# Performance work log

Hardware: AMD Instinct MI355X
Metric: run time of the kernel (lower is better)

## Reference

```python
import jax, jax.numpy as jnp
import numpy as np

DELTA = 0.2  # margin from __init__
EPS = 1e-8   # torch cosine_similarity eps


def setup_inputs() -> dict:
    key = jax.random.key(0)
    k1, k2, k3 = jax.random.split(key, 3)
    B, D, N = 4096, 1024, 8192
    return {
        "q": jax.random.normal(k1, (B, D), dtype=jnp.float32),
        "k": jax.random.normal(k2, (B, D), dtype=jnp.float32),
        "queue": jax.random.normal(k3, (N, D), dtype=jnp.float32),
    }


def _l2_normalize(x):
    # matches torch cosine_similarity clamping: norm clamped to eps
    n = jnp.maximum(jnp.linalg.norm(x, axis=-1, keepdims=True), EPS)
    return x / n


def reference(q, k, queue):
    qn = _l2_normalize(q)          # [B, D]
    kn = _l2_normalize(k)          # [B, D]
    queuen = _l2_normalize(queue)  # [N, D]
    pos = jnp.sum(qn * kn, axis=-1)                 # [B] cos(q_i, k_i)
    neg = jnp.einsum("bd,nd->bn", qn, queuen)       # [B, N] cos(q_i, queue_j)
    hinge = jax.nn.relu(DELTA - pos[:, None] + neg)  # [B, N]
    return jnp.sum(hinge)
```

## Files before the change

### kernel.cpp

```cpp
#include <hip/hip_runtime.h>

#define B_ROWS 4096
#define N_ROWS 8192
#define DDIM   1024
#define DELTA_M 0.2f
#define EPSF    1e-8f

#define BK3 32
#define NW  (DDIM / BK3)

typedef short bf16x8 __attribute__((ext_vector_type(8)));
typedef float f32x4 __attribute__((ext_vector_type(4)));

__device__ inline unsigned short f32_to_bf16(float f) {
    unsigned int u = __float_as_uint(f);
    u += 0x7FFFu + ((u >> 16) & 1u);
    return (unsigned short)(u >> 16);
}

__device__ inline void load_lds16(const void* g, void* l) {
    __builtin_amdgcn_global_load_lds(
        (const __attribute__((address_space(1))) void*)g,
        (__attribute__((address_space(3))) void*)l,
        16, 0, 0);
}

__global__ __launch_bounds__(256)
void norm_kernel(const float* __restrict__ q, const float* __restrict__ k,
                 const float* __restrict__ queue,
                 unsigned short* __restrict__ qn,
                 unsigned short* __restrict__ qun,
                 float* __restrict__ pos, float* __restrict__ out) {
    const int tid  = threadIdx.x;
    const int lane = tid & 63;
    const int wave = tid >> 6;
    const int row  = blockIdx.x * 4 + wave;
    if (blockIdx.x == 0 && tid == 0) *out = 0.f;

    if (row < B_ROWS) {
        const float4* qr = reinterpret_cast<const float4*>(q + (size_t)row * DDIM);
        const float4* kr = reinterpret_cast<const float4*>(k + (size_t)row * DDIM);
        float4 a[4], b[4];
        #pragma unroll
        for (int j = 0; j < 4; ++j) a[j] = qr[lane + j * 64];
        #pragma unroll
        for (int j = 0; j < 4; ++j) b[j] = kr[lane + j * 64];
        float s11 = 0.f, s22 = 0.f, s12 = 0.f;
        #pragma unroll
        for (int j = 0; j < 4; ++j) {
            s11 += a[j].x * a[j].x + a[j].y * a[j].y + a[j].z * a[j].z + a[j].w * a[j].w;
            s22 += b[j].x * b[j].x + b[j].y * b[j].y + b[j].z * b[j].z + b[j].w * b[j].w;
            s12 += a[j].x * b[j].x + a[j].y * b[j].y + a[j].z * b[j].z + a[j].w * b[j].w;
        }
        #pragma unroll
        for (int off = 1; off < 64; off <<= 1) {
            s11 += __shfl_xor(s11, off);
            s22 += __shfl_xor(s22, off);
            s12 += __shfl_xor(s12, off);
        }
        const float inv1 = 1.0f / fmaxf(sqrtf(s11), EPSF);
        const float inv2 = 1.0f / fmaxf(sqrtf(s22), EPSF);
        if (lane == 0) pos[row] = s12 * inv1 * inv2;
        ushort4* orow = reinterpret_cast<ushort4*>(qn + (size_t)row * DDIM);
        #pragma unroll
        for (int j = 0; j < 4; ++j) {
            ushort4 o;
            o.x = f32_to_bf16(a[j].x * inv1);
            o.y = f32_to_bf16(a[j].y * inv1);
            o.z = f32_to_bf16(a[j].z * inv1);
            o.w = f32_to_bf16(a[j].w * inv1);
            orow[lane + j * 64] = o;
        }
    } else {
        const int r2 = row - B_ROWS;
        const float4* qr = reinterpret_cast<const float4*>(queue + (size_t)r2 * DDIM);
        float4 a[4];
        #pragma unroll
        for (int j = 0; j < 4; ++j) a[j] = qr[lane + j * 64];
        float s11 = 0.f;
        #pragma unroll
        for (int j = 0; j < 4; ++j)
            s11 += a[j].x * a[j].x + a[j].y * a[j].y + a[j].z * a[j].z + a[j].w * a[j].w;
        #pragma unroll
        for (int off = 1; off < 64; off <<= 1) s11 += __shfl_xor(s11, off);
        const float inv1 = 1.0f / fmaxf(sqrtf(s11), EPSF);
        ushort4* orow = reinterpret_cast<ushort4*>(qun + (size_t)r2 * DDIM);
        #pragma unroll
        for (int j = 0; j < 4; ++j) {
            ushort4 o;
            o.x = f32_to_bf16(a[j].x * inv1);
            o.y = f32_to_bf16(a[j].y * inv1);
            o.z = f32_to_bf16(a[j].z * inv1);
            o.w = f32_to_bf16(a[j].w * inv1);
            orow[lane + j * 64] = o;
        }
    }
}

struct Frags { bf16x8 a[8]; bf16x8 b[4]; };

__device__ __forceinline__ void ld_frags(const unsigned char* buf, int aBase, int bBase,
                                         Frags& f) {
    #pragma unroll
    for (int fm = 0; fm < 8; ++fm)
        f.a[fm] = *reinterpret_cast<const bf16x8*>(&buf[aBase + fm * 1024]);
    #pragma unroll
    for (int fn = 0; fn < 4; ++fn)
        f.b[fn] = *reinterpret_cast<const bf16x8*>(&buf[16384 + bBase + fn * 1024]);
}

__device__ __forceinline__ void do_mfma(const Frags& f, f32x4 (&acc)[8][4]) {
    __builtin_amdgcn_s_setprio(1);
    #pragma unroll
    for (int fm = 0; fm < 8; ++fm)
        #pragma unroll
        for (int fn = 0; fn < 4; ++fn)
            acc[fm][fn] = __builtin_amdgcn_mfma_f32_16x16x32_bf16(
                f.a[fm], f.b[fn], acc[fm][fn], 0, 0, 0);
    __builtin_amdgcn_s_setprio(0);
}

__device__ __forceinline__ void stage(const unsigned short* sA0, const unsigned short* sA1,
                                      const unsigned short* sB0, const unsigned short* sB1,
                                      int k0, unsigned char* buf, int t16) {
    load_lds16(sA0 + k0, buf + t16);
    load_lds16(sA1 + k0, buf + 8192 + t16);
    load_lds16(sB0 + k0, buf + 16384 + t16);
    load_lds16(sB1 + k0, buf + 24576 + t16);
}

template<bool STG, int WE>
__device__ __forceinline__ void window(int T, unsigned char* lds,
    Frags& use, Frags& nxt,
    const unsigned short* sA0, const unsigned short* sA1,
    const unsigned short* sB0, const unsigned short* sB1,
    int aBase, int bBase, int t16, f32x4 (&acc)[8][4]) {

    ld_frags(lds + ((T + 1) % 3) * 32768, aBase, bBase, nxt);
    if (STG)
        stage(sA0, sA1, sB0, sB1, (T + 3) * BK3, lds + (T % 3) * 32768, t16);
    do_mfma(use, acc);
    if (WE == 4)      asm volatile("s_waitcnt vmcnt(4)" ::: "memory");
    else if (WE == 0) asm volatile("s_waitcnt vmcnt(0)" ::: "memory");
    asm volatile("s_waitcnt lgkmcnt(0)" ::: "memory");
    __builtin_amdgcn_sched_barrier(0);
    if (WE >= 0) __builtin_amdgcn_s_barrier();
}

__global__ __launch_bounds__(512, 2)
void gemm_hinge(const unsigned short* __restrict__ A,
                const unsigned short* __restrict__ Bq,
                const float* __restrict__ pos,
                float* __restrict__ out) {
    __shared__ __align__(16) unsigned char lds[98304];

    const int tid  = threadIdx.x;
    const int lane = tid & 63;
    const int wave = tid >> 6;

    const int bid = blockIdx.x;
    const int x   = bid & 7;
    const int idx = bid >> 3;
    const int bm = ((x & 1) * 8 + (idx & 7)) * 256;
    const int bn = ((x >> 1) * 8 + (idx >> 3)) * 256;

    const int wr = wave >> 2, wc = wave & 3;
    const int ln15 = lane & 15, kq = lane >> 4;
    const int kqoff = (kq * 16) ^ (((ln15 >> 1) & 3) << 4);
    const int aBase = wr * 8192 + ln15 * 64 + kqoff;
    const int bBase = wc * 4096 + ln15 * 64 + kqoff;

    const int t16 = tid * 16;
    const int d0 = t16, d1 = t16 + 8192;
    const int l0 = d0 ^ (((d0 >> 7) & 3) << 4);
    const int l1 = d1 ^ (((d1 >> 7) & 3) << 4);
    const int sr0 = l0 >> 6, sc0 = (l0 & 63) >> 1;
    const int sr1 = l1 >> 6, sc1 = (l1 & 63) >> 1;
    const unsigned short* sA0 = A  + (size_t)(bm + sr0) * DDIM + sc0;
    const unsigned short* sA1 = A  + (size_t)(bm + sr1) * DDIM + sc1;
    const unsigned short* sB0 = Bq + (size_t)(bn + sr0) * DDIM + sc0;
    const unsigned short* sB1 = Bq + (size_t)(bn + sr1) * DDIM + sc1;

    f32x4 acc[8][4];
    #pragma unroll
    for (int fm = 0; fm < 8; ++fm)
        #pragma unroll
        for (int fn = 0; fn < 4; ++fn)
            acc[fm][fn] = (f32x4){0.f, 0.f, 0.f, 0.f};

    Frags fA, fB;

    stage(sA0, sA1, sB0, sB1, 0,       lds,         t16);
    stage(sA0, sA1, sB0, sB1, BK3,     lds + 32768, t16);
    stage(sA0, sA1, sB0, sB1, 2 * BK3, lds + 65536, t16);
    asm volatile("s_waitcnt vmcnt(8)" ::: "memory");
    __builtin_amdgcn_sched_barrier(0);
    __builtin_amdgcn_s_barrier();
    ld_frags(lds, aBase, bBase, fA);
    asm volatile("s_waitcnt vmcnt(4) lgkmcnt(0)" ::: "memory");
    __builtin_amdgcn_sched_barrier(0);
    __builtin_amdgcn_s_barrier();

    #pragma unroll 1
    for (int T = 0; T < 28; T += 2) {
        window<true, 4>(T,     lds, fA, fB, sA0, sA1, sB0, sB1, aBase, bBase, t16, acc);
        window<true, 4>(T + 1, lds, fB, fA, sA0, sA1, sB0, sB1, aBase, bBase, t16, acc);
    }
    window<true,  4>(28, lds, fA, fB, sA0, sA1, sB0, sB1, aBase, bBase, t16, acc);
    window<false, 0>(29, lds, fB, fA, sA0, sA1, sB0, sB1, aBase, bBase, t16, acc);
    window<false,-1>(30, lds, fA, fB, sA0, sA1, sB0, sB1, aBase, bBase, t16, acc);
    do_mfma(fB, acc);

    float lsum = 0.f;
    #pragma unroll
    for (int fm = 0; fm < 8; ++fm) {
        const float4 p4 = *reinterpret_cast<const float4*>(
            pos + bm + wr * 128 + fm * 16 + kq * 4);
        const float pj[4] = {p4.x, p4.y, p4.z, p4.w};
        #pragma unroll
        for (int fn = 0; fn < 4; ++fn)
            #pragma unroll
            for (int j = 0; j < 4; ++j)
                lsum += fmaxf(DELTA_M - pj[j] + acc[fm][fn][j], 0.f);
    }
    #pragma unroll
    for (int off = 32; off; off >>= 1) lsum += __shfl_down(lsum, off);
    __syncthreads();
    float* red = reinterpret_cast<float*>(lds);
    if (lane == 0) red[wave] = lsum;
    __syncthreads();
    if (tid == 0) {
        float s = 0.f;
        #pragma unroll
        for (int w = 0; w < 8; ++w) s += red[w];
        atomicAdd(out, s);
    }
}

extern "C" void kernel_launch(void* const* d_in, const int* in_sizes, int n_in,
                              void* d_out, int out_size, void* d_ws, size_t ws_size,
                              hipStream_t stream) {
    const float* q     = (const float*)d_in[0];
    const float* k     = (const float*)d_in[1];
    const float* queue = (const float*)d_in[2];
    float* out = (float*)d_out;

    unsigned short* qn  = (unsigned short*)d_ws;
    unsigned short* qun = qn + (size_t)B_ROWS * DDIM;
    float* pos = (float*)(qun + (size_t)N_ROWS * DDIM);

    norm_kernel<<<(B_ROWS + N_ROWS) / 4, 256, 0, stream>>>(q, k, queue, qn, qun, pos, out);
    gemm_hinge<<<(B_ROWS / 256) * (N_ROWS / 256), 512, 0, stream>>>(qn, qun, pos, out);
}
```

Baseline: 155.4 us.

## Switch GEMM operands to FP8 with pre-tiled fragment layout from norm kernel

Result: faster. 148.1 us (-4.7%).

```diff
diff --git a/kernel.cpp b/kernel.cpp
--- a/kernel.cpp
+++ b/kernel.cpp
@@ -6,17 +6,11 @@
 #define DELTA_M 0.2f
 #define EPSF    1e-8f
 
-#define BK3 32
-#define NW  (DDIM / BK3)
-
-typedef short bf16x8 __attribute__((ext_vector_type(8)));
+#define NW 32
+#define PANEL (256 * DDIM)
+
 typedef float f32x4 __attribute__((ext_vector_type(4)));
-
-__device__ inline unsigned short f32_to_bf16(float f) {
-    unsigned int u = __float_as_uint(f);
-    u += 0x7FFFu + ((u >> 16) & 1u);
-    return (unsigned short)(u >> 16);
-}
+typedef unsigned long long u64;
 
 __device__ inline void load_lds16(const void* g, void* l) {
     __builtin_amdgcn_global_load_lds(
@@ -25,11 +19,17 @@
         16, 0, 0);
 }
 
+__device__ inline unsigned int pk4(float a, float b, float c, float d) {
+    int v = __builtin_amdgcn_cvt_pk_fp8_f32(a, b, 0, false);
+    v = __builtin_amdgcn_cvt_pk_fp8_f32(c, d, v, true);
+    return (unsigned int)v;
+}
+
 __global__ __launch_bounds__(256)
 void norm_kernel(const float* __restrict__ q, const float* __restrict__ k,
                  const float* __restrict__ queue,
-                 unsigned short* __restrict__ qn,
-                 unsigned short* __restrict__ qun,
+                 unsigned char* __restrict__ qn,
+                 unsigned char* __restrict__ qun,
                  float* __restrict__ pos, float* __restrict__ out) {
     const int tid  = threadIdx.x;
     const int lane = tid & 63;
@@ -42,9 +42,9 @@
         const float4* kr = reinterpret_cast<const float4*>(k + (size_t)row * DDIM);
         float4 a[4], b[4];
         #pragma unroll
-        for (int j = 0; j < 4; ++j) a[j] = qr[lane + j * 64];
-        #pragma unroll
-        for (int j = 0; j < 4; ++j) b[j] = kr[lane + j * 64];
+        for (int j = 0; j < 4; ++j) a[j] = qr[lane * 4 + j];
+        #pragma unroll
+        for (int j = 0; j < 4; ++j) b[j] = kr[lane * 4 + j];
         float s11 = 0.f, s22 = 0.f, s12 = 0.f;
         #pragma unroll
         for (int j = 0; j < 4; ++j) {
@@ -61,22 +61,23 @@
         const float inv1 = 1.0f / fmaxf(sqrtf(s11), EPSF);
         const float inv2 = 1.0f / fmaxf(sqrtf(s22), EPSF);
         if (lane == 0) pos[row] = s12 * inv1 * inv2;
-        ushort4* orow = reinterpret_cast<ushort4*>(qn + (size_t)row * DDIM);
-        #pragma unroll
-        for (int j = 0; j < 4; ++j) {
-            ushort4 o;
-            o.x = f32_to_bf16(a[j].x * inv1);
-            o.y = f32_to_bf16(a[j].y * inv1);
-            o.z = f32_to_bf16(a[j].z * inv1);
-            o.w = f32_to_bf16(a[j].w * inv1);
-            orow[lane + j * 64] = o;
-        }
+        u64 g0 = (u64)pk4(a[0].x * inv1, a[0].y * inv1, a[0].z * inv1, a[0].w * inv1)
+               | ((u64)pk4(a[1].x * inv1, a[1].y * inv1, a[1].z * inv1, a[1].w * inv1) << 32);
+        u64 g1 = (u64)pk4(a[2].x * inv1, a[2].y * inv1, a[2].z * inv1, a[2].w * inv1)
+               | ((u64)pk4(a[3].x * inv1, a[3].y * inv1, a[3].z * inv1, a[3].w * inv1) << 32);
+        const size_t base = (size_t)(row >> 8) * PANEL
+                          + (size_t)(lane >> 1) * 8192
+                          + (size_t)((row >> 4) & 15) * 512
+                          + (size_t)((lane & 1) * 2) * 128
+                          + (size_t)(row & 15) * 8;
+        *reinterpret_cast<u64*>(qn + base)       = g0;
+        *reinterpret_cast<u64*>(qn + base + 128) = g1;
     } else {
         const int r2 = row - B_ROWS;
         const float4* qr = reinterpret_cast<const float4*>(queue + (size_t)r2 * DDIM);
         float4 a[4];
         #pragma unroll
-        for (int j = 0; j < 4; ++j) a[j] = qr[lane + j * 64];
+        for (int j = 0; j < 4; ++j) a[j] = qr[lane * 4 + j];
         float s11 = 0.f;
         #pragma unroll
         for (int j = 0; j < 4; ++j)
@@ -84,29 +85,30 @@
         #pragma unroll
         for (int off = 1; off < 64; off <<= 1) s11 += __shfl_xor(s11, off);
         const float inv1 = 1.0f / fmaxf(sqrtf(s11), EPSF);
-        ushort4* orow = reinterpret_cast<ushort4*>(qun + (size_t)r2 * DDIM);
-        #pragma unroll
-        for (int j = 0; j < 4; ++j) {
-            ushort4 o;
-            o.x = f32_to_bf16(a[j].x * inv1);
-            o.y = f32_to_bf16(a[j].y * inv1);
-            o.z = f32_to_bf16(a[j].z * inv1);
-            o.w = f32_to_bf16(a[j].w * inv1);
-            orow[lane + j * 64] = o;
-        }
-    }
-}
-
-struct Frags { bf16x8 a[8]; bf16x8 b[4]; };
-
-__device__ __forceinline__ void ld_frags(const unsigned char* buf, int aBase, int bBase,
+        u64 g0 = (u64)pk4(a[0].x * inv1, a[0].y * inv1, a[0].z * inv1, a[0].w * inv1)
+               | ((u64)pk4(a[1].x * inv1, a[1].y * inv1, a[1].z * inv1, a[1].w * inv1) << 32);
+        u64 g1 = (u64)pk4(a[2].x * inv1, a[2].y * inv1, a[2].z * inv1, a[2].w * inv1)
+               | ((u64)pk4(a[3].x * inv1, a[3].y * inv1, a[3].z * inv1, a[3].w * inv1) << 32);
+        const size_t base = (size_t)(r2 >> 8) * PANEL
+                          + (size_t)(lane >> 1) * 8192
+                          + (size_t)((r2 >> 4) & 15) * 512
+                          + (size_t)((lane & 1) * 2) * 128
+                          + (size_t)(r2 & 15) * 8;
+        *reinterpret_cast<u64*>(qun + base)       = g0;
+        *reinterpret_cast<u64*>(qun + base + 128) = g1;
+    }
+}
+
+struct Frags { long long a[8]; long long b[4]; };
+
+__device__ __forceinline__ void ld_frags(const unsigned char* buf, int aOff, int bOff,
                                          Frags& f) {
     #pragma unroll
     for (int fm = 0; fm < 8; ++fm)
-        f.a[fm] = *reinterpret_cast<const bf16x8*>(&buf[aBase + fm * 1024]);
+        f.a[fm] = *reinterpret_cast<const long long*>(buf + aOff + fm * 512);
     #pragma unroll
     for (int fn = 0; fn < 4; ++fn)
-        f.b[fn] = *reinterpret_cast<const bf16x8*>(&buf[16384 + bBase + fn * 1024]);
+        f.b[fn] = *reinterpret_cast<const long long*>(buf + 8192 + bOff + fn * 512);
 }
 
 __device__ __forceinline__ void do_mfma(const Frags& f, f32x4 (&acc)[8][4]) {
@@ -115,32 +117,25 @@
     for (int fm = 0; fm < 8; ++fm)
         #pragma unroll
         for (int fn = 0; fn < 4; ++fn)
-            acc[fm][fn] = __builtin_amdgcn_mfma_f32_16x16x32_bf16(
+            acc[fm][fn] = __builtin_amdgcn_mfma_f32_16x16x32_fp8_fp8(
                 f.a[fm], f.b[fn], acc[fm][fn], 0, 0, 0);
     __builtin_amdgcn_s_setprio(0);
-}
-
-__device__ __forceinline__ void stage(const unsigned short* sA0, const unsigned short* sA1,
-                                      const unsigned short* sB0, const unsigned short* sB1,
-                                      int k0, unsigned char* buf, int t16) {
-    load_lds16(sA0 + k0, buf + t16);
-    load_lds16(sA1 + k0, buf + 8192 + t16);
-    load_lds16(sB0 + k0, buf + 16384 + t16);
-    load_lds16(sB1 + k0, buf + 24576 + t16);
 }
 
 template<bool STG, int WE>
 __device__ __forceinline__ void window(int T, unsigned char* lds,
     Frags& use, Frags& nxt,
-    const unsigned short* sA0, const unsigned short* sA1,
-    const unsigned short* sB0, const unsigned short* sB1,
-    int aBase, int bBase, int t16, f32x4 (&acc)[8][4]) {
-
-    ld_frags(lds + ((T + 1) % 3) * 32768, aBase, bBase, nxt);
-    if (STG)
-        stage(sA0, sA1, sB0, sB1, (T + 3) * BK3, lds + (T % 3) * 32768, t16);
+    const unsigned char* srcA, const unsigned char* srcB,
+    int aOff, int bOff, int t16, f32x4 (&acc)[8][4]) {
+
+    ld_frags(lds + ((T + 1) % 3) * 16384, aOff, bOff, nxt);
+    if (STG) {
+        unsigned char* buf = lds + (T % 3) * 16384;
+        load_lds16(srcA + (T + 3) * 8192, buf + t16);
+        load_lds16(srcB + (T + 3) * 8192, buf + 8192 + t16);
+    }
     do_mfma(use, acc);
-    if (WE == 4)      asm volatile("s_waitcnt vmcnt(4)" ::: "memory");
+    if (WE == 2)      asm volatile("s_waitcnt vmcnt(2)" ::: "memory");
     else if (WE == 0) asm volatile("s_waitcnt vmcnt(0)" ::: "memory");
     asm volatile("s_waitcnt lgkmcnt(0)" ::: "memory");
     __builtin_amdgcn_sched_barrier(0);
@@ -148,11 +143,11 @@
 }
 
 __global__ __launch_bounds__(512, 2)
-void gemm_hinge(const unsigned short* __restrict__ A,
-                const unsigned short* __restrict__ Bq,
+void gemm_hinge(const unsigned char* __restrict__ A,
+                const unsigned char* __restrict__ Bq,
                 const float* __restrict__ pos,
                 float* __restrict__ out) {
-    __shared__ __align__(16) unsigned char lds[98304];
+    __shared__ __align__(16) unsigned char lds[49152];
 
     const int tid  = threadIdx.x;
     const int lane = tid & 63;
@@ -161,25 +156,16 @@
     const int bid = blockIdx.x;
     const int x   = bid & 7;
     const int idx = bid >> 3;
-    const int bm = ((x & 1) * 8 + (idx & 7)) * 256;
-    const int bn = ((x >> 1) * 8 + (idx >> 3)) * 256;
+    const int bm = ((x & 1) * 8 + (idx & 7));
+    const int bn = ((x >> 1) * 8 + (idx >> 3));
 
     const int wr = wave >> 2, wc = wave & 3;
-    const int ln15 = lane & 15, kq = lane >> 4;
-    const int kqoff = (kq * 16) ^ (((ln15 >> 1) & 3) << 4);
-    const int aBase = wr * 8192 + ln15 * 64 + kqoff;
-    const int bBase = wc * 4096 + ln15 * 64 + kqoff;
+    const int aOff = wr * 4096 + lane * 8;
+    const int bOff = wc * 2048 + lane * 8;
 
     const int t16 = tid * 16;
-    const int d0 = t16, d1 = t16 + 8192;
-    const int l0 = d0 ^ (((d0 >> 7) & 3) << 4);
-    const int l1 = d1 ^ (((d1 >> 7) & 3) << 4);
-    const int sr0 = l0 >> 6, sc0 = (l0 & 63) >> 1;
-    const int sr1 = l1 >> 6, sc1 = (l1 & 63) >> 1;
-    const unsigned short* sA0 = A  + (size_t)(bm + sr0) * DDIM + sc0;
-    const unsigned short* sA1 = A  + (size_t)(bm + sr1) * DDIM + sc1;
-    const unsigned short* sB0 = Bq + (size_t)(bn + sr0) * DDIM + sc0;
-    const unsigned short* sB1 = Bq + (size_t)(bn + sr1) * DDIM + sc1;
+    const unsigned char* srcA = A  + (size_t)bm * PANEL + t16;
+    const unsigned char* srcB = Bq + (size_t)bn * PANEL + t16;
 
     f32x4 acc[8][4];
     #pragma unroll
@@ -190,32 +176,34 @@
 
     Frags fA, fB;
 
-    stage(sA0, sA1, sB0, sB1, 0,       lds,         t16);
-    stage(sA0, sA1, sB0, sB1, BK3,     lds + 32768, t16);
-    stage(sA0, sA1, sB0, sB1, 2 * BK3, lds + 65536, t16);
-    asm volatile("s_waitcnt vmcnt(8)" ::: "memory");
+    #pragma unroll
+    for (int t = 0; t < 3; ++t) {
+        load_lds16(srcA + t * 8192, lds + t * 16384 + t16);
+        load_lds16(srcB + t * 8192, lds + t * 16384 + 8192 + t16);
+    }
+    asm volatile("s_waitcnt vmcnt(4)" ::: "memory");
     __builtin_amdgcn_sched_barrier(0);
     __builtin_amdgcn_s_barrier();
-    ld_frags(lds, aBase, bBase, fA);
-    asm volatile("s_waitcnt vmcnt(4) lgkmcnt(0)" ::: "memory");
+    ld_frags(lds, aOff, bOff, fA);
+    asm volatile("s_waitcnt vmcnt(2) lgkmcnt(0)" ::: "memory");
     __builtin_amdgcn_sched_barrier(0);
     __builtin_amdgcn_s_barrier();
 
     #pragma unroll 1
     for (int T = 0; T < 28; T += 2) {
-        window<true, 4>(T,     lds, fA, fB, sA0, sA1, sB0, sB1, aBase, bBase, t16, acc);
-        window<true, 4>(T + 1, lds, fB, fA, sA0, sA1, sB0, sB1, aBase, bBase, t16, acc);
-    }
-    window<true,  4>(28, lds, fA, fB, sA0, sA1, sB0, sB1, aBase, bBase, t16, acc);
-    window<false, 0>(29, lds, fB, fA, sA0, sA1, sB0, sB1, aBase, bBase, t16, acc);
-    window<false,-1>(30, lds, fA, fB, sA0, sA1, sB0, sB1, aBase, bBase, t16, acc);
+        window<true, 2>(T,     lds, fA, fB, srcA, srcB, aOff, bOff, t16, acc);
+        window<true, 2>(T + 1, lds, fB, fA, srcA, srcB, aOff, bOff, t16, acc);
+    }
+    window<true,  2>(28, lds, fA, fB, srcA, srcB, aOff, bOff, t16, acc);
+    window<false, 0>(29, lds, fB, fA, srcA, srcB, aOff, bOff, t16, acc);
+    window<false,-1>(30, lds, fA, fB, srcA, srcB, aOff, bOff, t16, acc);
     do_mfma(fB, acc);
 
     float lsum = 0.f;
     #pragma unroll
     for (int fm = 0; fm < 8; ++fm) {
         const float4 p4 = *reinterpret_cast<const float4*>(
-            pos + bm + wr * 128 + fm * 16 + kq * 4);
+            pos + bm * 256 + wr * 128 + fm * 16 + (lane >> 4) * 4);
         const float pj[4] = {p4.x, p4.y, p4.z, p4.w};
         #pragma unroll
         for (int fn = 0; fn < 4; ++fn)
@@ -245,8 +233,8 @@
     const float* queue = (const float*)d_in[2];
     float* out = (float*)d_out;
 
-    unsigned short* qn  = (unsigned short*)d_ws;
-    unsigned short* qun = qn + (size_t)B_ROWS * DDIM;
+    unsigned char* qn  = (unsigned char*)d_ws;
+    unsigned char* qun = qn + (size_t)B_ROWS * DDIM;
     float* pos = (float*)(qun + (size_t)N_ROWS * DDIM);
 
     norm_kernel<<<(B_ROWS + N_ROWS) / 4, 256, 0, stream>>>(q, k, queue, qn, qun, pos, out);
```
